# Optimization experiments

Hardware: AMD Instinct MI355X
Metric: run time of the kernel (lower is better)

## Reference

```python
import jax, jax.numpy as jnp
import numpy as np

DIM, HEADS, HEAD_DIM = 1024, 16, 64
B, L, S = 4, 2048, 2048
EPS = 1e-5
NEG_INF = -1e9


def rms_norm(x, w):
    # x: [..., d]; normalize over last dim, scale by learned weight w [d]
    var = jnp.mean(jnp.square(x), axis=-1, keepdims=True)
    return x * jax.lax.rsqrt(var + EPS) * w


def setup_inputs() -> dict:
    key = jax.random.key(0)
    ks = jax.random.split(key, 9)
    hd = HEADS * HEAD_DIM
    scale = 1.0 / np.sqrt(DIM)
    return {
        "q": jax.random.normal(ks[0], (B, L, DIM), dtype=jnp.float32),
        "kv": jax.random.normal(ks[1], (B, S, DIM), dtype=jnp.float32),
        "x_seqlens": jax.random.randint(ks[2], (B,), 1, S + 1, dtype=jnp.int32),
        "Wq": jax.random.normal(ks[3], (DIM, hd), dtype=jnp.float32) * scale,
        "Wk": jax.random.normal(ks[4], (DIM, hd), dtype=jnp.float32) * scale,
        "Wv": jax.random.normal(ks[5], (DIM, hd), dtype=jnp.float32) * scale,
        "Wo": jax.random.normal(ks[6], (hd, DIM), dtype=jnp.float32) * (1.0 / np.sqrt(hd)),
        "q_norm_w": jnp.ones((HEAD_DIM,), dtype=jnp.float32),
        "k_norm_w": jnp.ones((HEAD_DIM,), dtype=jnp.float32),
    }


def reference(q, kv, x_seqlens, Wq, Wk, Wv, Wo, q_norm_w, k_norm_w):
    b, l, _ = q.shape
    s = kv.shape[1]
    # QKV projections -> [b, h, n, d]
    qh = (q @ Wq).reshape(b, l, HEADS, HEAD_DIM).transpose(0, 2, 1, 3)
    kh = (kv @ Wk).reshape(b, s, HEADS, HEAD_DIM).transpose(0, 2, 1, 3)
    vh = (kv @ Wv).reshape(b, s, HEADS, HEAD_DIM).transpose(0, 2, 1, 3)
    # per-head RMSNorm on q and k
    qh = rms_norm(qh, q_norm_w)
    kh = rms_norm(kh, k_norm_w)
    # dense padding mask [b, 1, 1, s]: True where kv position is valid
    mask = (jnp.arange(s, dtype=jnp.int32)[None, :] < x_seqlens[:, None])[:, None, None, :]
    # scaled dot-product attention (math path: full score matrix)
    scores = jnp.einsum("bhld,bhsd->bhls", qh, kh) * (1.0 / np.sqrt(HEAD_DIM))
    scores = jnp.where(mask, scores, NEG_INF)
    attn = jax.nn.softmax(scores, axis=-1)
    o = jnp.einsum("bhls,bhsd->bhld", attn, vh)  # [b, h, l, d]
    o = o.transpose(0, 2, 1, 3).reshape(b, l, HEADS * HEAD_DIM)
    return o @ Wo
```

## Files before the change

kernel.cpp:

```cpp
#include <hip/hip_runtime.h>
#include <hip/hip_bf16.h>
#include <stdint.h>

#define BB 4
#define LL 2048
#define SS 2048
#define DIMM 1024
#define HH 16
#define HD 64
#define NHD 1024

typedef __bf16 bf16_t;
typedef __bf16 bf16x8 __attribute__((ext_vector_type(8)));
typedef __bf16 bf16x4 __attribute__((ext_vector_type(4)));
typedef float f32x4 __attribute__((ext_vector_type(4)));

#define GLDS16(g, l) __builtin_amdgcn_global_load_lds( \
    (const __attribute__((address_space(1))) void*)(g), \
    (__attribute__((address_space(3))) void*)(l), 16, 0, 0)

#define FENCED_BARRIER() do {                    \
    asm volatile("" ::: "memory");               \
    __builtin_amdgcn_s_barrier();                \
    asm volatile("" ::: "memory");               \
    __builtin_amdgcn_sched_barrier(0);           \
  } while (0)

__global__ __launch_bounds__(256) void cvt_all(const float* __restrict__ q,
                                               const float* __restrict__ kv,
                                               bf16_t* __restrict__ Aq,
                                               bf16_t* __restrict__ Akv) {
  const int bi = blockIdx.x;
  const float* in = (bi < 4096) ? q : kv;
  bf16_t* out = (bi < 4096) ? Aq : Akv;
  size_t i = ((size_t)(bi & 4095) * 256 + threadIdx.x) * 8;
  const f32x4* p = (const f32x4*)(in + i);
  f32x4 a = p[0], b = p[1];
  bf16x8 o;
#pragma unroll
  for (int j = 0; j < 4; ++j) { o[j] = (bf16_t)a[j]; o[4 + j] = (bf16_t)b[j]; }
  *(bf16x8*)(out + i) = o;
}

__global__ __launch_bounds__(256) void transpose_all(
    const float* __restrict__ W0, const float* __restrict__ W1,
    const float* __restrict__ W2, const float* __restrict__ W3,
    bf16_t* __restrict__ O0, bf16_t* __restrict__ O1,
    bf16_t* __restrict__ O2, bf16_t* __restrict__ O3) {
  const float* in = (blockIdx.z == 0) ? W0 : (blockIdx.z == 1) ? W1
                    : (blockIdx.z == 2) ? W2 : W3;
  bf16_t* out = (blockIdx.z == 0) ? O0 : (blockIdx.z == 1) ? O1
                : (blockIdx.z == 2) ? O2 : O3;
  __shared__ float tile[64][65];
  const int r0 = blockIdx.y * 64, c0 = blockIdx.x * 64;
  const int tr = threadIdx.x >> 2;
  const int tc4 = (threadIdx.x & 3) * 16;
#pragma unroll
  for (int i = 0; i < 4; ++i) {
    f32x4 v = *(const f32x4*)&in[(size_t)(r0 + tr) * 1024 + c0 + tc4 + i * 4];
    tile[tr][tc4 + i * 4 + 0] = v.x;
    tile[tr][tc4 + i * 4 + 1] = v.y;
    tile[tr][tc4 + i * 4 + 2] = v.z;
    tile[tr][tc4 + i * 4 + 3] = v.w;
  }
  __syncthreads();
#pragma unroll
  for (int i = 0; i < 2; ++i) {
    bf16x8 o;
#pragma unroll
    for (int j = 0; j < 8; ++j) o[j] = (bf16_t)tile[tc4 + i * 8 + j][tr];
    *(bf16x8*)&out[(size_t)(c0 + tr) * 1024 + r0 + tc4 + i * 8] = o;
  }
}

__global__ __launch_bounds__(256) void proj_qkv(
    const bf16_t* __restrict__ Aq, const bf16_t* __restrict__ Akv,
    const bf16_t* __restrict__ WqT, const bf16_t* __restrict__ WkT,
    const bf16_t* __restrict__ WvT,
    bf16_t* __restrict__ Qb, bf16_t* __restrict__ Kb, bf16_t* __restrict__ Vt,
    const float* __restrict__ qw, const float* __restrict__ kw, float qscale) {
  __shared__ bf16_t As[2][4096];
  __shared__ bf16_t Bs[2][4096];
  const int nt = blockIdx.x;
  const int mode = (nt < 8) ? 0 : (nt < 16 ? 1 : 2);
  const bf16_t* A  = (mode == 0) ? Aq : Akv;
  const bf16_t* Bt = (mode == 0) ? WqT : (mode == 1 ? WkT : WvT);
  const int n0 = (nt & 7) * 128;
  const int m0 = blockIdx.y * 128;
  const int K = 1024;
  const int tid = threadIdx.x, lane = tid & 63, w = tid >> 6;
  const int wm = (w >> 1) * 64, wn = (w & 1) * 64;
  const int fr = lane & 15, fg = lane >> 4;
  f32x4 acc[4][4] = {};

  auto stage = [&](int kt, int bi) {
    const int kb = kt * 32;
#pragma unroll
    for (int j = 0; j < 2; ++j) {
      int e = (j * 4 + w) * 512 + lane * 8;
      int r = e >> 5, c = e & 31;
      GLDS16(A  + (size_t)(m0 + r) * K + kb + c, &As[bi][(j * 4 + w) * 512]);
      GLDS16(Bt + (size_t)(n0 + r) * K + kb + c, &Bs[bi][(j * 4 + w) * 512]);
    }
  };

  stage(0, 0);
  int cur = 0;
  for (int kt = 0; kt < 32; ++kt) {
    if (kt + 1 < 32) {
      stage(kt + 1, cur ^ 1);
      asm volatile("s_waitcnt vmcnt(4)" ::: "memory");
    } else {
      asm volatile("s_waitcnt vmcnt(0)" ::: "memory");
    }
    FENCED_BARRIER();
    bf16x8 a[4], b[4];
#pragma unroll
    for (int m = 0; m < 4; ++m) a[m] = *(const bf16x8*)&As[cur][(wm + m * 16 + fr) * 32 + fg * 8];
#pragma unroll
    for (int n = 0; n < 4; ++n) b[n] = *(const bf16x8*)&Bs[cur][(wn + n * 16 + fr) * 32 + fg * 8];
    __builtin_amdgcn_s_setprio(1);
#pragma unroll
    for (int m = 0; m < 4; ++m)
#pragma unroll
      for (int n = 0; n < 4; ++n)
        acc[m][n] = __builtin_amdgcn_mfma_f32_16x16x32_bf16(a[m], b[n], acc[m][n], 0, 0, 0);
    __builtin_amdgcn_s_setprio(0);
    FENCED_BARRIER();
    cur ^= 1;
  }

  if (mode <= 1) {
    const float* nw = (mode == 0) ? qw : kw;
    const float ps = (mode == 0) ? qscale : 1.0f;
    bf16_t* Cb = (mode == 0) ? Qb : Kb;
    float w4[4];
#pragma unroll
    for (int n = 0; n < 4; ++n) w4[n] = nw[n * 16 + fr] * ps;
#pragma unroll
    for (int m = 0; m < 4; ++m) {
      float ss[4];
#pragma unroll
      for (int j = 0; j < 4; ++j) {
        ss[j] = 0.f;
#pragma unroll
        for (int n = 0; n < 4; ++n) ss[j] += acc[m][n][j] * acc[m][n][j];
      }
#pragma unroll
      for (int d = 1; d < 16; d <<= 1)
#pragma unroll
        for (int j = 0; j < 4; ++j) ss[j] += __shfl_xor(ss[j], d);
      float rs[4];
#pragma unroll
      for (int j = 0; j < 4; ++j) rs[j] = rsqrtf(ss[j] * (1.f / 64.f) + 1e-5f);
#pragma unroll
      for (int n = 0; n < 4; ++n)
#pragma unroll
        for (int j = 0; j < 4; ++j) {
          size_t row = (size_t)m0 + wm + m * 16 + fg * 4 + j;
          size_t col = (size_t)n0 + wn + n * 16 + fr;
          Cb[row * NHD + col] = (bf16_t)(acc[m][n][j] * rs[j] * w4[n]);
        }
    }
  } else {
#pragma unroll
    for (int m = 0; m < 4; ++m) {
      int r = m0 + wm + m * 16 + fg * 4;
      int bb_ = r >> 11, s0 = r & 2047;
#pragma unroll
      for (int n = 0; n < 4; ++n) {
        int cc = n0 + wn + n * 16 + fr;
        int hh_ = cc >> 6, dd = cc & 63;
        bf16x4 pk;
#pragma unroll
        for (int j = 0; j < 4; ++j) pk[j] = (bf16_t)acc[m][n][j];
        *(bf16x4*)&Vt[(((size_t)bb_ * 16 + hh_) * 64 + dd) * 2048 + s0] = pk;
      }
    }
  }
}

__global__ __launch_bounds__(256) void gemm_out(const bf16_t* __restrict__ A,
                                                const bf16_t* __restrict__ Bt,
                                                float* __restrict__ Cout) {
  __shared__ bf16_t As[2][4096];
  __shared__ bf16_t Bs[2][4096];
  const int K = 1024, N = 1024;
  const int tid = threadIdx.x, lane = tid & 63, w = tid >> 6;
  const int m0 = blockIdx.y * 128, n0 = blockIdx.x * 128;
  const int wm = (w >> 1) * 64, wn = (w & 1) * 64;
  const int fr = lane & 15, fg = lane >> 4;
  f32x4 acc[4][4] = {};

  auto stage = [&](int kt, int bi) {
    const int kb = kt * 32;
#pragma unroll
    for (int j = 0; j < 2; ++j) {
      int e = (j * 4 + w) * 512 + lane * 8;
      int r = e >> 5, c = e & 31;
      GLDS16(A  + (size_t)(m0 + r) * K + kb + c, &As[bi][(j * 4 + w) * 512]);
      GLDS16(Bt + (size_t)(n0 + r) * K + kb + c, &Bs[bi][(j * 4 + w) * 512]);
    }
  };

  stage(0, 0);
  int cur = 0;
  for (int kt = 0; kt < 32; ++kt) {
    if (kt + 1 < 32) {
      stage(kt + 1, cur ^ 1);
      asm volatile("s_waitcnt vmcnt(4)" ::: "memory");
    } else {
      asm volatile("s_waitcnt vmcnt(0)" ::: "memory");
    }
    FENCED_BARRIER();
    bf16x8 a[4], b[4];
#pragma unroll
    for (int m = 0; m < 4; ++m) a[m] = *(const bf16x8*)&As[cur][(wm + m * 16 + fr) * 32 + fg * 8];
#pragma unroll
    for (int n = 0; n < 4; ++n) b[n] = *(const bf16x8*)&Bs[cur][(wn + n * 16 + fr) * 32 + fg * 8];
    __builtin_amdgcn_s_setprio(1);
#pragma unroll
    for (int m = 0; m < 4; ++m)
#pragma unroll
      for (int n = 0; n < 4; ++n)
        acc[m][n] = __builtin_amdgcn_mfma_f32_16x16x32_bf16(a[m], b[n], acc[m][n], 0, 0, 0);
    __builtin_amdgcn_s_setprio(0);
    FENCED_BARRIER();
    cur ^= 1;
  }
#pragma unroll
  for (int m = 0; m < 4; ++m)
#pragma unroll
    for (int n = 0; n < 4; ++n)
#pragma unroll
      for (int j = 0; j < 4; ++j) {
        size_t row = (size_t)m0 + wm + m * 16 + fg * 4 + j;
        size_t col = (size_t)n0 + wn + n * 16 + fr;
        Cout[row * N + col] = acc[m][n][j];
      }
}

__global__ __launch_bounds__(256, 3) void attn64(const bf16_t* __restrict__ Qb,
                                                 const bf16_t* __restrict__ Kb,
                                                 const bf16_t* __restrict__ Vtg,
                                                 bf16_t* __restrict__ Ob,
                                                 const int* __restrict__ seqlens) {
  __shared__ bf16_t Kl[2][4096];
  __shared__ bf16_t Vl[2][4096];
  __shared__ bf16_t Pl[8192];
  const int tid = threadIdx.x, lane = tid & 63, w = tid >> 6;
  const int fr = lane & 15, fg = lane >> 4;
  const int qt = blockIdx.x, bh = blockIdx.y;
  const int b = bh >> 4, h = bh & 15;
  const int seqlen = seqlens[b];
  const int ntiles = (seqlen + 63) >> 6;
  bf16_t* Pw = &Pl[w * 2048];

  const bf16_t* qp = Qb + ((size_t)b * LL + qt * 128 + w * 32 + fr) * NHD + h * 64;
  bf16x8 qf[2][2];
#pragma unroll
  for (int qs = 0; qs < 2; ++qs) {
    qf[qs][0] = *(const bf16x8*)&qp[(size_t)qs * 16 * NHD + fg * 8];
    qf[qs][1] = *(const bf16x8*)&qp[(size_t)qs * 16 * NHD + 32 + fg * 8];
  }
  asm volatile("s_waitcnt vmcnt(0)" ::: "memory");

  const bf16_t* Kg = Kb + (size_t)b * SS * NHD + h * 64;
  const bf16_t* Vg = Vtg + ((size_t)(b * 16 + h)) * 64 * SS;

  auto stage = [&](int t, int bi) {
#pragma unroll
    for (int c = 0; c < 2; ++c) {
      const int ro = (w * 2 + c) * 8 + (lane >> 3);
      const int cs = ((lane & 7) ^ (ro & 7)) * 8;
      GLDS16(Kg + (size_t)(t * 64 + ro) * NHD + cs, &Kl[bi][(w * 2 + c) * 512]);
      GLDS16(Vg + (size_t)ro * SS + t * 64 + cs, &Vl[bi][(w * 2 + c) * 512]);
    }
  };

  bf16x8 vones;
#pragma unroll
  for (int i = 0; i < 8; ++i) vones[i] = (bf16_t)1.0f;

  f32x4 oacc[2][4] = {};
  f32x4 lacc[2] = {};
  const float M0 = 12.0f;

  auto softmax_strip = [&](f32x4 (&s)[4], int qs, int t) {
    if (t == ntiles - 1 && (seqlen & 63)) {
#pragma unroll
      for (int n = 0; n < 4; ++n) {
        bool valid = (t * 64 + n * 16 + fr) < seqlen;
#pragma unroll
        for (int j = 0; j < 4; ++j) s[n][j] = valid ? s[n][j] : -1e30f;
      }
    }
#pragma unroll
    for (int n = 0; n < 4; ++n)
#pragma unroll
      for (int j = 0; j < 4; ++j) s[n][j] = __builtin_exp2f(s[n][j] - M0);
#pragma unroll
    for (int n = 0; n < 4; ++n)
#pragma unroll
      for (int j = 0; j < 4; ++j) {
        const int prow = qs * 16 + fg * 4 + j;
        const int pcol = n * 16 + fr;
        Pw[prow * 64 + (((pcol >> 3) ^ (prow & 7)) * 8) + (pcol & 7)] =
            (bf16_t)s[n][j];
      }
  };

  stage(0, 0);
  int cur = 0;
  for (int t = 0; t < ntiles; ++t) {
    if (t + 1 < ntiles) {
      stage(t + 1, cur ^ 1);
      asm volatile("s_waitcnt vmcnt(4)" ::: "memory");
    } else {
      asm volatile("s_waitcnt vmcnt(0)" ::: "memory");
    }
    FENCED_BARRIER();

    f32x4 s0[4] = {}, s1[4] = {};
    __builtin_amdgcn_s_setprio(1);
#pragma unroll
    for (int n = 0; n < 4; ++n) {
      const int rr = n * 16 + fr;
      bf16x8 kf0 = *(const bf16x8*)&Kl[cur][rr * 64 + ((fg ^ (rr & 7)) * 8)];
      bf16x8 kf1 = *(const bf16x8*)&Kl[cur][rr * 64 + (((fg + 4) ^ (rr & 7)) * 8)];
      s0[n] = __builtin_amdgcn_mfma_f32_16x16x32_bf16(qf[0][0], kf0, s0[n], 0, 0, 0);
      s0[n] = __builtin_amdgcn_mfma_f32_16x16x32_bf16(qf[0][1], kf1, s0[n], 0, 0, 0);
      s1[n] = __builtin_amdgcn_mfma_f32_16x16x32_bf16(qf[1][0], kf0, s1[n], 0, 0, 0);
      s1[n] = __builtin_amdgcn_mfma_f32_16x16x32_bf16(qf[1][1], kf1, s1[n], 0, 0, 0);
    }
    __builtin_amdgcn_s_setprio(0);

    softmax_strip(s0, 0, t);
    softmax_strip(s1, 1, t);

    asm volatile("s_waitcnt lgkmcnt(0)" ::: "memory");
    __builtin_amdgcn_sched_barrier(0);

    __builtin_amdgcn_s_setprio(1);
#pragma unroll
    for (int ks = 0; ks < 2; ++ks) {
      const int pr0 = fr, pr1 = 16 + fr;
      bf16x8 pa0 = *(const bf16x8*)&Pw[pr0 * 64 + (((ks * 4 + fg) ^ (pr0 & 7)) * 8)];
      bf16x8 pa1 = *(const bf16x8*)&Pw[pr1 * 64 + (((ks * 4 + fg) ^ (pr1 & 7)) * 8)];
#pragma unroll
      for (int n = 0; n < 4; ++n) {
        const int rr = n * 16 + fr;
        bf16x8 vf = *(const bf16x8*)&Vl[cur][rr * 64 + (((ks * 4 + fg) ^ (rr & 7)) * 8)];
        oacc[0][n] = __builtin_amdgcn_mfma_f32_16x16x32_bf16(pa0, vf, oacc[0][n], 0, 0, 0);
        oacc[1][n] = __builtin_amdgcn_mfma_f32_16x16x32_bf16(pa1, vf, oacc[1][n], 0, 0, 0);
      }
      lacc[0] = __builtin_amdgcn_mfma_f32_16x16x32_bf16(pa0, vones, lacc[0], 0, 0, 0);
      lacc[1] = __builtin_amdgcn_mfma_f32_16x16x32_bf16(pa1, vones, lacc[1], 0, 0, 0);
    }
    __builtin_amdgcn_s_setprio(0);
    FENCED_BARRIER();
    cur ^= 1;
  }

#pragma unroll
  for (int qs = 0; qs < 2; ++qs) {
    float inv[4];
#pragma unroll
    for (int j = 0; j < 4; ++j) inv[j] = __builtin_amdgcn_rcpf(lacc[qs][j]);
#pragma unroll
    for (int n = 0; n < 4; ++n)
#pragma unroll
      for (int j = 0; j < 4; ++j) {
        size_t row = (size_t)b * LL + qt * 128 + w * 32 + qs * 16 + fg * 4 + j;
        Ob[row * NHD + h * 64 + n * 16 + fr] = (bf16_t)(oacc[qs][n][j] * inv[j]);
      }
  }
}

extern "C" void kernel_launch(void* const* d_in, const int* in_sizes, int n_in,
                              void* d_out, int out_size, void* d_ws, size_t ws_size,
                              hipStream_t stream) {
  const float* q   = (const float*)d_in[0];
  const float* kv  = (const float*)d_in[1];
  const int* seqlens = (const int*)d_in[2];
  const float* Wq = (const float*)d_in[3];
  const float* Wk = (const float*)d_in[4];
  const float* Wv = (const float*)d_in[5];
  const float* Wo = (const float*)d_in[6];
  const float* qw = (const float*)d_in[7];
  const float* kw = (const float*)d_in[8];

  char* ws = (char*)d_ws;
  const size_t MB = 1 << 20;
  bf16_t* Aq  = (bf16_t*)(ws + 0 * MB);
  bf16_t* Akv = (bf16_t*)(ws + 16 * MB);
  bf16_t* WqT = (bf16_t*)(ws + 32 * MB);
  bf16_t* WkT = (bf16_t*)(ws + 34 * MB);
  bf16_t* WvT = (bf16_t*)(ws + 36 * MB);
  bf16_t* WoT = (bf16_t*)(ws + 38 * MB);
  bf16_t* Qb  = (bf16_t*)(ws + 40 * MB);
  bf16_t* Kb  = (bf16_t*)(ws + 56 * MB);
  bf16_t* Vt  = (bf16_t*)(ws + 72 * MB);

  const float QSCALE = 0.125f * 1.44269504088896f;

  cvt_all<<<8192, 256, 0, stream>>>(q, kv, Aq, Akv);
  dim3 tg(16, 16, 4);
  transpose_all<<<tg, 256, 0, stream>>>(Wq, Wk, Wv, Wo, WqT, WkT, WvT, WoT);
  dim3 pg(24, 64);
  proj_qkv<<<pg, 256, 0, stream>>>(Aq, Akv, WqT, WkT, WvT, Qb, Kb, Vt,
                                   qw, kw, QSCALE);
  dim3 ag(LL / 128, BB * HH);
  attn64<<<ag, 256, 0, stream>>>(Qb, Kb, Vt, Aq, seqlens);
  dim3 og(8, 64);
  gemm_out<<<og, 256, 0, stream>>>(Aq, WoT, (float*)d_out);
}
```

Baseline: 196.4 us.

## Enlarge QKV projection tiles to 256x256 with swizzled LDS and pipelined fragment loads

Reworks the QKV projection GEMM from 128x128 tiles with 4 waves to 256x256 tiles with 8 waves, a K-step of 64, and an XOR-swizzled LDS layout to avoid bank conflicts. A-fragment LDS reads are double-buffered across four sub-steps so they overlap with MFMA work. This is meant to raise arithmetic intensity and cut global and LDS traffic per flop. The cost is 128KB of LDS per block, one block per CU, more barriers per K-step, and a grid of only 384 blocks, which may leave the device under-filled.

After: 193.4 us. About the same (-1.5%).

```diff
diff --git a/kernel.cpp b/kernel.cpp
--- a/kernel.cpp
+++ b/kernel.cpp
@@ -25,6 +25,8 @@
     asm volatile("" ::: "memory");               \
     __builtin_amdgcn_sched_barrier(0);           \
   } while (0)
+
+#define SWZ(o) ((o) ^ ((((o) >> 7) & 7) << 4))
 
 __global__ __launch_bounds__(256) void cvt_all(const float* __restrict__ q,
                                                const float* __restrict__ kv,
@@ -73,60 +75,94 @@
   }
 }
 
-__global__ __launch_bounds__(256) void proj_qkv(
+__global__ __launch_bounds__(512, 1) void proj_qkv(
     const bf16_t* __restrict__ Aq, const bf16_t* __restrict__ Akv,
     const bf16_t* __restrict__ WqT, const bf16_t* __restrict__ WkT,
     const bf16_t* __restrict__ WvT,
     bf16_t* __restrict__ Qb, bf16_t* __restrict__ Kb, bf16_t* __restrict__ Vt,
     const float* __restrict__ qw, const float* __restrict__ kw, float qscale) {
-  __shared__ bf16_t As[2][4096];
-  __shared__ bf16_t Bs[2][4096];
+  __shared__ bf16_t Lds[2][4][8192];
   const int nt = blockIdx.x;
-  const int mode = (nt < 8) ? 0 : (nt < 16 ? 1 : 2);
+  const int mode = nt >> 2;
   const bf16_t* A  = (mode == 0) ? Aq : Akv;
   const bf16_t* Bt = (mode == 0) ? WqT : (mode == 1 ? WkT : WvT);
-  const int n0 = (nt & 7) * 128;
-  const int m0 = blockIdx.y * 128;
-  const int K = 1024;
+  const int n0 = (nt & 3) * 256;
+  const int m0 = blockIdx.y * 256;
   const int tid = threadIdx.x, lane = tid & 63, w = tid >> 6;
-  const int wm = (w >> 1) * 64, wn = (w & 1) * 64;
+  const int wr = w >> 2, wc = w & 3;
   const int fr = lane & 15, fg = lane >> 4;
-  f32x4 acc[4][4] = {};
-
-  auto stage = [&](int kt, int bi) {
-    const int kb = kt * 32;
-#pragma unroll
-    for (int j = 0; j < 2; ++j) {
-      int e = (j * 4 + w) * 512 + lane * 8;
-      int r = e >> 5, c = e & 31;
-      GLDS16(A  + (size_t)(m0 + r) * K + kb + c, &As[bi][(j * 4 + w) * 512]);
-      GLDS16(Bt + (size_t)(n0 + r) * K + kb + c, &Bs[bi][(j * 4 + w) * 512]);
+  f32x4 acc[8][4] = {};
+
+  auto stageKT = [&](int kt, int d) {
+#pragma unroll
+    for (int ht = 0; ht < 4; ++ht) {
+#pragma unroll
+      for (int c = 0; c < 2; ++c) {
+        const int o = (c * 512 + tid) * 16;
+        const int eff = SWZ(o);
+        const int rl = eff >> 7, ce = (eff & 127) >> 1;
+        const bf16_t* src = (ht < 2)
+            ? A  + (size_t)(m0 + ht * 128 + rl) * 1024 + kt * 64 + ce
+            : Bt + (size_t)(n0 + (ht - 2) * 128 + rl) * 1024 + kt * 64 + ce;
+        GLDS16(src, &Lds[d][ht][c * 4096 + w * 512]);
+      }
     }
   };
 
-  stage(0, 0);
+  stageKT(0, 0);
   int cur = 0;
-  for (int kt = 0; kt < 32; ++kt) {
-    if (kt + 1 < 32) {
-      stage(kt + 1, cur ^ 1);
-      asm volatile("s_waitcnt vmcnt(4)" ::: "memory");
+  for (int kt = 0; kt < 16; ++kt) {
+    if (kt + 1 < 16) {
+      stageKT(kt + 1, cur ^ 1);
+      asm volatile("s_waitcnt vmcnt(8)" ::: "memory");
     } else {
       asm volatile("s_waitcnt vmcnt(0)" ::: "memory");
     }
     FENCED_BARRIER();
-    bf16x8 a[4], b[4];
-#pragma unroll
-    for (int m = 0; m < 4; ++m) a[m] = *(const bf16x8*)&As[cur][(wm + m * 16 + fr) * 32 + fg * 8];
-#pragma unroll
-    for (int n = 0; n < 4; ++n) b[n] = *(const bf16x8*)&Bs[cur][(wn + n * 16 + fr) * 32 + fg * 8];
-    __builtin_amdgcn_s_setprio(1);
-#pragma unroll
-    for (int m = 0; m < 4; ++m)
-#pragma unroll
-      for (int n = 0; n < 4; ++n)
-        acc[m][n] = __builtin_amdgcn_mfma_f32_16x16x32_bf16(a[m], b[n], acc[m][n], 0, 0, 0);
-    __builtin_amdgcn_s_setprio(0);
-    FENCED_BARRIER();
+
+    bf16x8 bfr[4][2];
+#pragma unroll
+    for (int n = 0; n < 4; ++n)
+#pragma unroll
+      for (int ks = 0; ks < 2; ++ks) {
+        const int o = ((wc & 1) * 64 + n * 16 + fr) * 128 + ks * 64 + fg * 16;
+        bfr[n][ks] = *(const bf16x8*)&Lds[cur][2 + (wc >> 1)][SWZ(o) >> 1];
+      }
+    bf16x8 af[2][4];
+#pragma unroll
+    for (int ks = 0; ks < 2; ++ks)
+#pragma unroll
+      for (int m2 = 0; m2 < 2; ++m2) {
+        const int o = (m2 * 16 + fr) * 128 + ks * 64 + fg * 16;
+        af[0][m2 * 2 + ks] = *(const bf16x8*)&Lds[cur][wr][SWZ(o) >> 1];
+      }
+
+#pragma unroll
+    for (int q = 0; q < 4; ++q) {
+      asm volatile("s_waitcnt lgkmcnt(0)" ::: "memory");
+      __builtin_amdgcn_sched_barrier(0);
+      if (q < 3) {
+#pragma unroll
+        for (int ks = 0; ks < 2; ++ks)
+#pragma unroll
+          for (int m2 = 0; m2 < 2; ++m2) {
+            const int o = ((q + 1) * 32 + m2 * 16 + fr) * 128 + ks * 64 + fg * 16;
+            af[(q + 1) & 1][m2 * 2 + ks] =
+                *(const bf16x8*)&Lds[cur][wr][SWZ(o) >> 1];
+          }
+      }
+      __builtin_amdgcn_s_setprio(1);
+#pragma unroll
+      for (int m2 = 0; m2 < 2; ++m2)
+#pragma unroll
+        for (int n = 0; n < 4; ++n)
+#pragma unroll
+          for (int ks = 0; ks < 2; ++ks)
+            acc[q * 2 + m2][n] = __builtin_amdgcn_mfma_f32_16x16x32_bf16(
+                af[q & 1][m2 * 2 + ks], bfr[n][ks], acc[q * 2 + m2][n], 0, 0, 0);
+      __builtin_amdgcn_s_setprio(0);
+      FENCED_BARRIER();
+    }
     cur ^= 1;
   }
 
@@ -138,7 +174,7 @@
 #pragma unroll
     for (int n = 0; n < 4; ++n) w4[n] = nw[n * 16 + fr] * ps;
 #pragma unroll
-    for (int m = 0; m < 4; ++m) {
+    for (int m = 0; m < 8; ++m) {
       float ss[4];
 #pragma unroll
       for (int j = 0; j < 4; ++j) {
@@ -157,19 +193,19 @@
       for (int n = 0; n < 4; ++n)
 #pragma unroll
         for (int j = 0; j < 4; ++j) {
-          size_t row = (size_t)m0 + wm + m * 16 + fg * 4 + j;
-          size_t col = (size_t)n0 + wn + n * 16 + fr;
+          size_t row = (size_t)m0 + wr * 128 + m * 16 + fg * 4 + j;
+          size_t col = (size_t)n0 + wc * 64 + n * 16 + fr;
           Cb[row * NHD + col] = (bf16_t)(acc[m][n][j] * rs[j] * w4[n]);
         }
     }
   } else {
 #pragma unroll
-    for (int m = 0; m < 4; ++m) {
-      int r = m0 + wm + m * 16 + fg * 4;
+    for (int m = 0; m < 8; ++m) {
+      int r = m0 + wr * 128 + m * 16 + fg * 4;
       int bb_ = r >> 11, s0 = r & 2047;
 #pragma unroll
       for (int n = 0; n < 4; ++n) {
-        int cc = n0 + wn + n * 16 + fr;
+        int cc = n0 + wc * 64 + n * 16 + fr;
         int hh_ = cc >> 6, dd = cc & 63;
         bf16x4 pk;
 #pragma unroll
@@ -407,8 +443,8 @@
   cvt_all<<<8192, 256, 0, stream>>>(q, kv, Aq, Akv);
   dim3 tg(16, 16, 4);
   transpose_all<<<tg, 256, 0, stream>>>(Wq, Wk, Wv, Wo, WqT, WkT, WvT, WoT);
-  dim3 pg(24, 64);
-  proj_qkv<<<pg, 256, 0, stream>>>(Aq, Akv, WqT, WkT, WvT, Qb, Kb, Vt,
+  dim3 pg(12, 32);
+  proj_qkv<<<pg, 512, 0, stream>>>(Aq, Akv, WqT, WkT, WvT, Qb, Kb, Vt,
                                    qw, kw, QSCALE);
   dim3 ag(LL / 128, BB * HH);
   attn64<<<ag, 256, 0, stream>>>(Qb, Kb, Vt, Aq, seqlens);
```
